# Kernel optimization log

Hardware: AMD Instinct MI355X
Metric: run time of the kernel (lower is better)

Reference implementation:

```python
import jax, jax.numpy as jnp
import numpy as np

HIDDEN_DIM = 2048
CODE_DIM = 256
CODEBOOK_SIZE = 512
FC_DIMS = [1024, 512]
BATCH = 16384
EPS = 1e-5
NEG_SLOPE = 0.01  # PyTorch LeakyReLU default


def _linear_init(key, fan_in, fan_out):
    # kaiming_uniform_(a=sqrt(3)) ~= U(-1/sqrt(fan_in), 1/sqrt(fan_in)) scaled; use uniform bound
    bound = 1.0 / np.sqrt(fan_in)
    return jax.random.uniform(key, (fan_in, fan_out), jnp.float32, -bound, bound)


def setup_inputs() -> dict:
    key = jax.random.key(0)
    ks = jax.random.split(key, 16)
    h = jax.random.normal(ks[0], (BATCH, HIDDEN_DIM), jnp.float32)
    # encoder: Linear(2048->1024, no bias), BN, LReLU, Linear(1024->512, no bias), BN, LReLU, Linear(512->256, bias)
    enc_w1 = _linear_init(ks[1], HIDDEN_DIM, FC_DIMS[0])
    enc_bn1_g = jnp.ones((FC_DIMS[0],), jnp.float32)
    enc_bn1_b = jnp.zeros((FC_DIMS[0],), jnp.float32)
    enc_w2 = _linear_init(ks[2], FC_DIMS[0], FC_DIMS[1])
    enc_bn2_g = jnp.ones((FC_DIMS[1],), jnp.float32)
    enc_bn2_b = jnp.zeros((FC_DIMS[1],), jnp.float32)
    enc_w3 = _linear_init(ks[3], FC_DIMS[1], CODE_DIM)
    enc_b3 = jax.random.uniform(ks[4], (CODE_DIM,), jnp.float32, -1/np.sqrt(FC_DIMS[1]), 1/np.sqrt(FC_DIMS[1]))
    # codebook: NearestEmbed weight shape (code_dim, codebook_size)
    codebook = jax.random.normal(ks[5], (CODE_DIM, CODEBOOK_SIZE), jnp.float32)
    # decoder: Linear(256->512, no bias), BN, LReLU, Linear(512->1024, no bias), BN, LReLU, Linear(1024->2048, bias)
    dec_w1 = _linear_init(ks[6], CODE_DIM, FC_DIMS[1])
    dec_bn1_g = jnp.ones((FC_DIMS[1],), jnp.float32)
    dec_bn1_b = jnp.zeros((FC_DIMS[1],), jnp.float32)
    dec_w2 = _linear_init(ks[7], FC_DIMS[1], FC_DIMS[0])
    dec_bn2_g = jnp.ones((FC_DIMS[0],), jnp.float32)
    dec_bn2_b = jnp.zeros((FC_DIMS[0],), jnp.float32)
    dec_w3 = _linear_init(ks[8], FC_DIMS[0], HIDDEN_DIM)
    dec_b3 = jax.random.uniform(ks[9], (HIDDEN_DIM,), jnp.float32, -1/np.sqrt(FC_DIMS[0]), 1/np.sqrt(FC_DIMS[0]))
    return dict(h=h, enc_w1=enc_w1, enc_bn1_g=enc_bn1_g, enc_bn1_b=enc_bn1_b,
                enc_w2=enc_w2, enc_bn2_g=enc_bn2_g, enc_bn2_b=enc_bn2_b,
                enc_w3=enc_w3, enc_b3=enc_b3, codebook=codebook,
                dec_w1=dec_w1, dec_bn1_g=dec_bn1_g, dec_bn1_b=dec_bn1_b,
                dec_w2=dec_w2, dec_bn2_g=dec_bn2_g, dec_bn2_b=dec_bn2_b,
                dec_w3=dec_w3, dec_b3=dec_b3)


def _bn(x, g, b):
    # BatchNorm1d, training mode: biased batch variance, eps=1e-5
    mu = jnp.mean(x, axis=0)
    var = jnp.var(x, axis=0)
    return (x - mu) * jax.lax.rsqrt(var + EPS) * g + b


def _lrelu(x):
    return jnp.where(x >= 0, x, NEG_SLOPE * x)


def _quantize(z_e, codebook):
    # nearest codebook entry; codebook is [code_dim, K]
    # dist[b,k] = ||z_e[b] - codebook[:,k]||^2 (expanded, drop constant ||z||^2 for argmin? keep full for clarity)
    d = (jnp.sum(z_e * z_e, axis=1, keepdims=True)
         - 2.0 * (z_e @ codebook)
         + jnp.sum(codebook * codebook, axis=0)[None, :])  # [B, K]
    idx = jnp.argmin(d, axis=1)  # [B]
    z_q = codebook.T[idx]        # [B, code_dim]
    return z_q, idx


def reference(h, enc_w1, enc_bn1_g, enc_bn1_b, enc_w2, enc_bn2_g, enc_bn2_b,
              enc_w3, enc_b3, codebook,
              dec_w1, dec_bn1_g, dec_bn1_b, dec_w2, dec_bn2_g, dec_bn2_b,
              dec_w3, dec_b3):
    # encoder
    x = _lrelu(_bn(h @ enc_w1, enc_bn1_g, enc_bn1_b))
    x = _lrelu(_bn(x @ enc_w2, enc_bn2_g, enc_bn2_b))
    z_e = x @ enc_w3 + enc_b3  # [B, code_dim]
    # nearest-embed quantization with straight-through estimator
    z_q_raw, code_indices = _quantize(z_e, codebook)
    z_q = z_e + jax.lax.stop_gradient(z_q_raw - z_e)
    # decoder
    y = _lrelu(_bn(z_q @ dec_w1, dec_bn1_g, dec_bn1_b))
    y = _lrelu(_bn(y @ dec_w2, dec_bn2_g, dec_bn2_b))
    h_recon = y @ dec_w3 + dec_b3  # [B, hidden_dim]
    return z_e, z_q, h_recon, code_indices
```

## Files before the change

kernel.cpp:

```cpp
#include <hip/hip_runtime.h>
#include <hip/hip_fp16.h>
#include <cstdint>
#include <cstddef>

typedef _Float16 f16;
typedef _Float16 half8 __attribute__((ext_vector_type(8)));
typedef _Float16 half4 __attribute__((ext_vector_type(4)));
typedef float floatx4 __attribute__((ext_vector_type(4)));

static constexpr size_t NB  = 16384;
static constexpr size_t DH  = 2048;
static constexpr size_t F1  = 1024;
static constexpr size_t F2  = 512;
static constexpr size_t CD  = 256;
static constexpr size_t KCB = 512;

static constexpr size_t ZE_OFF  = 0;
static constexpr size_t ZQ_OFF  = NB * CD;
static constexpr size_t HR_OFF  = 2 * NB * CD;
static constexpr size_t IDX_OFF = 2 * NB * CD + NB * DH;

static constexpr size_t O_HH   = 0;
static constexpr size_t O_HL   = O_HH + NB * DH * 2;
static constexpr size_t R1_END = O_HL + NB * DH * 2;

static constexpr size_t R_X1H = 0;
static constexpr size_t R_X1L = NB * F1 * 2;
static constexpr size_t R_X2F = 2 * NB * F1 * 2;
static constexpr size_t R_X2H = R_X2F + NB * F2 * 4;
static constexpr size_t R_X2L = R_X2H + NB * F2 * 2;
static constexpr size_t R_Y1F = 0;
static constexpr size_t R_Y1H = NB * F2 * 4;
static constexpr size_t R_Y2H = 0;

static constexpr size_t O_W1H = R1_END;
static constexpr size_t O_W1L = O_W1H + F1 * DH * 2;
static constexpr size_t O_W2H = O_W1L + F1 * DH * 2;
static constexpr size_t O_W2L = O_W2H + F2 * F1 * 2;
static constexpr size_t O_W3H = O_W2L + F2 * F1 * 2;
static constexpr size_t O_W3L = O_W3H + CD * F2 * 2;
static constexpr size_t O_CBH = O_W3L + CD * F2 * 2;
static constexpr size_t O_CBL = O_CBH + KCB * CD * 2;
static constexpr size_t O_DW1 = O_CBL + KCB * CD * 2;
static constexpr size_t O_DW2 = O_DW1 + F2 * CD * 2;
static constexpr size_t O_DW3 = O_DW2 + F1 * F2 * 2;
static constexpr size_t O_SUM = O_DW3 + DH * F1 * 2;
static constexpr size_t O_SQ  = O_SUM + 4 * 1024 * 8;
static constexpr size_t O_SC  = O_SQ + 4 * 1024 * 8;
static constexpr size_t O_SH  = O_SC + 4 * 1024 * 4;
static constexpr size_t O_CN  = O_SH + 4 * 1024 * 4;
static constexpr size_t R2    = (O_CN + 4096 + 255) & ~(size_t)255;
static constexpr size_t R2_X1F = R2;
static constexpr size_t R2_ZEH = R2;
static constexpr size_t R2_ZEL = R2 + NB * CD * 2;
static constexpr size_t R2_S   = R2 + 2 * NB * CD * 2;
static constexpr size_t R2_ZQH = R2_S + NB * KCB * 4;
static constexpr size_t R2_Y2F = R2;

#define GLLDS(src, dst)                                                          \
    __builtin_amdgcn_global_load_lds(                                            \
        (const __attribute__((address_space(1))) void*)(src),                    \
        (__attribute__((address_space(3))) void*)(dst), 16, 0, 0)

#define VMCNT(n)  asm volatile("s_waitcnt vmcnt(" #n ")" ::: "memory")
#define LGKMCNT0  asm volatile("s_waitcnt lgkmcnt(0)" ::: "memory")

__device__ __forceinline__ void xcd_tile(int gx, int BM, int& row0, int& col0)
{
    int id = blockIdx.x + gx * blockIdx.y;
    const int nwg = gx * gridDim.y;
    id = (id & 7) * (nwg >> 3) + (id >> 3);
    row0 = (id % gx) * BM;
    col0 = (id / gx) * 256;
}

template<int MW, bool BIAS, bool STATS, bool WSPLIT>
__global__ __launch_bounds__(512)
void gemm3_t(const f16* __restrict__ Ah_, const f16* __restrict__ Al_,
             const f16* __restrict__ Bh_, const f16* __restrict__ Bl_,
             float* __restrict__ C, const float* __restrict__ bias,
             double* __restrict__ ssum, double* __restrict__ ssq,
             f16* __restrict__ zeh, f16* __restrict__ zel,
             int M, int N, int K)
{
    constexpr int BM = MW * 32;
    __shared__ f16 lds[2][2][16384];
    const int tid  = threadIdx.x;
    const int lane = tid & 63;
    const int w    = tid >> 6;
    const int wr   = w >> 2, wn = w & 3;
    int row0, col0;
    xcd_tile(gridDim.x, BM, row0, col0);

    const int rr8 = lane >> 3;
    const int p   = (lane & 7) ^ rr8;
    const int rr  = w * 32 + rr8;
    const int arr = rr & (BM - 1);
    const f16* srcH = (p < 4) ? (Ah_ + (size_t)(row0 + arr) * K + p * 8)
                              : (Bh_ + (size_t)(col0 + rr) * K + (p - 4) * 8);
    const f16* srcL = (p < 4) ? (Al_ + (size_t)(row0 + arr) * K + p * 8)
                              : (Bl_ + (size_t)(col0 + rr) * K + (p - 4) * 8);
    const int dstBase = w * 32 * 64;
    const int KT = K >> 5;

    floatx4 acc[MW][4];
#pragma unroll
    for (int m = 0; m < MW; ++m)
#pragma unroll
        for (int n = 0; n < 4; ++n)
#pragma unroll
            for (int j = 0; j < 4; ++j) acc[m][n][j] = 0.f;

    const int l15 = lane & 15;
    const int sA  = lane >> 4;

#pragma unroll
    for (int j = 0; j < 4; ++j)
        GLLDS(srcH + (size_t)j * 8 * K, &lds[0][0][dstBase + j * 512]);
#pragma unroll
    for (int j = 0; j < 4; ++j)
        GLLDS(srcL + (size_t)j * 8 * K, &lds[0][1][dstBase + j * 512]);
    VMCNT(4);
    __builtin_amdgcn_s_barrier();

    half8 afh[MW], afl[MW], bfh[4], bfl[4];

    for (int kt = 0; kt < KT; ++kt) {
        const int cur = kt & 1, nxt = cur ^ 1;
        const int koff = (kt + 1 < KT ? kt + 1 : kt) << 5;
        const f16* plH = lds[cur][0];
        const f16* plL = lds[cur][1];

#pragma unroll
        for (int m = 0; m < MW; ++m) {
            const int rA = wr * (MW * 16) + m * 16 + l15;
            afh[m] = *(const half8*)(plH + rA * 64 + (((sA) ^ (rA & 7)) << 3));
        }
#pragma unroll
        for (int n = 0; n < 4; ++n) {
            const int rB = wn * 64 + n * 16 + l15;
            bfh[n] = *(const half8*)(plH + rB * 64 + (((4 + sA) ^ (rB & 7)) << 3));
        }
#pragma unroll
        for (int j = 0; j < 4; ++j)
            GLLDS(srcH + (size_t)j * 8 * K + koff, &lds[nxt][0][dstBase + j * 512]);
        LGKMCNT0;
        __builtin_amdgcn_sched_barrier(0);
        __builtin_amdgcn_s_setprio(1);
#pragma unroll
        for (int m = 0; m < MW; ++m)
#pragma unroll
            for (int n = 0; n < 4; ++n)
                acc[m][n] = __builtin_amdgcn_mfma_f32_16x16x32_f16(afh[m], bfh[n], acc[m][n], 0, 0, 0);
        __builtin_amdgcn_s_setprio(0);
        VMCNT(4);
        __builtin_amdgcn_s_barrier();

#pragma unroll
        for (int n = 0; n < 4; ++n) {
            const int rB = wn * 64 + n * 16 + l15;
            bfl[n] = *(const half8*)(plL + rB * 64 + (((4 + sA) ^ (rB & 7)) << 3));
        }
#pragma unroll
        for (int m = 0; m < MW; ++m) {
            const int rA = wr * (MW * 16) + m * 16 + l15;
            afl[m] = *(const half8*)(plL + rA * 64 + (((sA) ^ (rA & 7)) << 3));
        }
#pragma unroll
        for (int j = 0; j < 4; ++j)
            GLLDS(srcL + (size_t)j * 8 * K + koff, &lds[nxt][1][dstBase + j * 512]);
        LGKMCNT0;
        __builtin_amdgcn_sched_barrier(0);
        __builtin_amdgcn_s_setprio(1);
#pragma unroll
        for (int m = 0; m < MW; ++m)
#pragma unroll
            for (int n = 0; n < 4; ++n)
                acc[m][n] = __builtin_amdgcn_mfma_f32_16x16x32_f16(afh[m], bfl[n], acc[m][n], 0, 0, 0);
#pragma unroll
        for (int m = 0; m < MW; ++m)
#pragma unroll
            for (int n = 0; n < 4; ++n)
                acc[m][n] = __builtin_amdgcn_mfma_f32_16x16x32_f16(afl[m], bfh[n], acc[m][n], 0, 0, 0);
        __builtin_amdgcn_s_setprio(0);
        VMCNT(4);
        __builtin_amdgcn_s_barrier();
    }
    VMCNT(0);

    const int cb0 = col0 + wn * 64;
    const int rb0 = row0 + wr * (MW * 16) + (lane >> 4) * 4;
#pragma unroll
    for (int n = 0; n < 4; ++n) {
        const int col = cb0 + n * 16 + l15;
        const float bv = BIAS ? bias[col] : 0.f;
        double sd = 0.0, sq = 0.0;
#pragma unroll
        for (int m = 0; m < MW; ++m) {
            const int row = rb0 + m * 16;
#pragma unroll
            for (int j = 0; j < 4; ++j) {
                const float v = acc[m][n][j] + bv;
                const size_t o = (size_t)(row + j) * N + col;
                C[o] = v;
                if (WSPLIT) {
                    const f16 hv = (f16)v;
                    zeh[o] = hv;
                    zel[o] = (f16)(v - (float)hv);
                }
                if (STATS) { sd += (double)v; sq += (double)v * (double)v; }
            }
        }
        if (STATS) {
            sd += __shfl_xor(sd, 16);
            sd += __shfl_xor(sd, 32);
            sq += __shfl_xor(sq, 16);
            sq += __shfl_xor(sq, 32);
            if (lane < 16) {
                atomicAdd(ssum + col, sd);
                atomicAdd(ssq + col, sq);
            }
        }
    }
}

template<int MW, bool BIAS, bool STATS>
__global__ __launch_bounds__(512)
void gemm1_t(const f16* __restrict__ A_, const f16* __restrict__ B_,
             float* __restrict__ C, const float* __restrict__ bias,
             double* __restrict__ ssum, double* __restrict__ ssq,
             int M, int N, int K)
{
    constexpr int BM = MW * 32;
    __shared__ f16 lds[3][16384];
    const int tid  = threadIdx.x;
    const int lane = tid & 63;
    const int w    = tid >> 6;
    const int wr   = w >> 2, wn = w & 3;
    int row0, col0;
    xcd_tile(gridDim.x, BM, row0, col0);

    const int rr8 = lane >> 3;
    const int p   = (lane & 7) ^ rr8;
    const int rr  = w * 32 + rr8;
    const int arr = rr & (BM - 1);
    const f16* srcH = (p < 4) ? (A_ + (size_t)(row0 + arr) * K + p * 8)
                              : (B_ + (size_t)(col0 + rr) * K + (p - 4) * 8);
    const int dstBase = w * 32 * 64;
    const int KT = K >> 5;

    floatx4 acc[MW][4];
#pragma unroll
    for (int m = 0; m < MW; ++m)
#pragma unroll
        for (int n = 0; n < 4; ++n)
#pragma unroll
            for (int j = 0; j < 4; ++j) acc[m][n][j] = 0.f;

    const int l15 = lane & 15;
    const int sA  = lane >> 4;

#pragma unroll
    for (int j = 0; j < 4; ++j)
        GLLDS(srcH + (size_t)j * 8 * K, &lds[0][dstBase + j * 512]);
    {
        const int k1 = (KT > 1 ? 1 : 0) << 5;
#pragma unroll
        for (int j = 0; j < 4; ++j)
            GLLDS(srcH + (size_t)j * 8 * K + k1, &lds[1][dstBase + j * 512]);
    }
    VMCNT(4);
    __builtin_amdgcn_s_barrier();

    half8 afh[MW], bfh[4];

    for (int kt = 0; kt < KT; ++kt) {
        const int cur = kt % 3, tgt = (kt + 2) % 3;
        const int koff = (kt + 2 < KT ? kt + 2 : KT - 1) << 5;
        const f16* plH = lds[cur];

#pragma unroll
        for (int m = 0; m < MW; ++m) {
            const int rA = wr * (MW * 16) + m * 16 + l15;
            afh[m] = *(const half8*)(plH + rA * 64 + (((sA) ^ (rA & 7)) << 3));
        }
#pragma unroll
        for (int n = 0; n < 4; ++n) {
            const int rB = wn * 64 + n * 16 + l15;
            bfh[n] = *(const half8*)(plH + rB * 64 + (((4 + sA) ^ (rB & 7)) << 3));
        }
#pragma unroll
        for (int j = 0; j < 4; ++j)
            GLLDS(srcH + (size_t)j * 8 * K + koff, &lds[tgt][dstBase + j * 512]);
        LGKMCNT0;
        __builtin_amdgcn_sched_barrier(0);
        __builtin_amdgcn_s_setprio(1);
#pragma unroll
        for (int m = 0; m < MW; ++m)
#pragma unroll
            for (int n = 0; n < 4; ++n)
                acc[m][n] = __builtin_amdgcn_mfma_f32_16x16x32_f16(afh[m], bfh[n], acc[m][n], 0, 0, 0);
        __builtin_amdgcn_s_setprio(0);
        VMCNT(4);
        __builtin_amdgcn_s_barrier();
    }
    VMCNT(0);

    const int cb0 = col0 + wn * 64;
    const int rb0 = row0 + wr * (MW * 16) + (lane >> 4) * 4;
#pragma unroll
    for (int n = 0; n < 4; ++n) {
        const int col = cb0 + n * 16 + l15;
        const float bv = BIAS ? bias[col] : 0.f;
        double sd = 0.0, sq = 0.0;
#pragma unroll
        for (int m = 0; m < MW; ++m) {
            const int row = rb0 + m * 16;
#pragma unroll
            for (int j = 0; j < 4; ++j) {
                const float v = acc[m][n][j] + bv;
                C[(size_t)(row + j) * N + col] = v;
                if (STATS) { sd += (double)v; sq += (double)v * (double)v; }
            }
        }
        if (STATS) {
            sd += __shfl_xor(sd, 16);
            sd += __shfl_xor(sd, 32);
            sq += __shfl_xor(sq, 16);
            sq += __shfl_xor(sq, 32);
            if (lane < 16) {
                atomicAdd(ssum + col, sd);
                atomicAdd(ssq + col, sq);
            }
        }
    }
}

__global__ void split_f32(const float* __restrict__ X, f16* __restrict__ hi,
                          f16* __restrict__ lo, size_t n4)
{
    const size_t stride = (size_t)gridDim.x * blockDim.x;
    for (size_t i = (size_t)blockIdx.x * blockDim.x + threadIdx.x; i < n4; i += stride) {
        const floatx4 x = ((const floatx4*)X)[i];
        half4 h, l;
#pragma unroll
        for (int j = 0; j < 4; ++j) {
            const float v = x[j];
            const f16 hv = (f16)v;
            h[j] = hv;
            l[j] = (f16)(v - (float)hv);
        }
        ((half4*)hi)[i] = h;
        ((half4*)lo)[i] = l;
    }
}

template<bool SPLIT>
__global__ void bn_apply(const float* __restrict__ X, const float* __restrict__ scale,
                         const float* __restrict__ shift, f16* __restrict__ Yhi,
                         f16* __restrict__ Ylo, size_t n4, int Nmask)
{
    const size_t stride = (size_t)gridDim.x * blockDim.x;
    for (size_t i = (size_t)blockIdx.x * blockDim.x + threadIdx.x; i < n4; i += stride) {
        const floatx4 x = ((const floatx4*)X)[i];
        const int col = (int)((i * 4) & (size_t)Nmask);
        half4 h, l;
#pragma unroll
        for (int j = 0; j < 4; ++j) {
            float v = x[j] * scale[col + j] + shift[col + j];
            v = v >= 0.f ? v : 0.01f * v;
            const f16 hv = (f16)v;
            h[j] = hv;
            if (SPLIT) l[j] = (f16)(v - (float)hv);
        }
        ((half4*)Yhi)[i] = h;
        if (SPLIT) ((half4*)Ylo)[i] = l;
    }
}

__global__ void bn_finalize(const double* __restrict__ ssum, const double* __restrict__ ssq,
                            const float* __restrict__ g, const float* __restrict__ b,
                            float* __restrict__ scale, float* __restrict__ shift, int N)
{
    const int j = blockIdx.x * blockDim.x + threadIdx.x;
    if (j < N) {
        const double inv = 1.0 / (double)NB;
        const double mean = ssum[j] * inv;
        const double var  = ssq[j] * inv - mean * mean;
        const double sc   = (double)g[j] / sqrt(var + 1e-5);
        scale[j] = (float)sc;
        shift[j] = (float)((double)b[j] - mean * sc);
    }
}

template<bool SPLIT>
__global__ void transpose_split(const float* __restrict__ W, f16* __restrict__ Thi,
                                f16* __restrict__ Tlo, int K, int N)
{
    __shared__ float tile[32][33];
    const int x = threadIdx.x;
    const int y = threadIdx.y;
    const int nt = blockIdx.x * 32;
    const int kt = blockIdx.y * 32;
#pragma unroll
    for (int i = 0; i < 32; i += 8)
        tile[y + i][x] = W[(size_t)(kt + y + i) * N + nt + x];
    __syncthreads();
#pragma unroll
    for (int i = 0; i < 32; i += 8) {
        const float v = tile[x][y + i];
        const size_t o = (size_t)(nt + y + i) * K + kt + x;
        const f16 hv = (f16)v;
        Thi[o] = hv;
        if (SPLIT) Tlo[o] = (f16)(v - (float)hv);
    }
}

__global__ void cnorm_kernel(const float* __restrict__ cb, float* __restrict__ cn)
{
    const int k = blockIdx.x * blockDim.x + threadIdx.x;
    if (k < (int)KCB) {
        double s = 0.0;
        for (int d = 0; d < (int)CD; ++d) {
            const float v = cb[(size_t)d * KCB + k];
            s += (double)v * v;
        }
        cn[k] = (float)s;
    }
}

__global__ void argmin_gather(const float* __restrict__ S, const float* __restrict__ cn,
                              const float* __restrict__ cb, float* __restrict__ zq,
                              float* __restrict__ idx_out, f16* __restrict__ zqh)
{
    const int lane = threadIdx.x & 63;
    const int row  = blockIdx.x * 4 + (threadIdx.x >> 6);
    const float* Sr = S + (size_t)row * KCB;
    float best = 3.4e38f;
    int bi = 0;
#pragma unroll
    for (int i = 0; i < 8; ++i) {
        const int k = lane + 64 * i;
        const float d = cn[k] - 2.f * Sr[k];
        if (d < best) { best = d; bi = k; }
    }
#pragma unroll
    for (int off = 32; off > 0; off >>= 1) {
        const float ob = __shfl_xor(best, off);
        const int   oi = __shfl_xor(bi, off);
        if (ob < best || (ob == best && oi < bi)) { best = ob; bi = oi; }
    }
    if (lane == 0) idx_out[row] = (float)bi;
#pragma unroll
    for (int i = 0; i < 4; ++i) {
        const int d = lane + 64 * i;
        const float v = cb[(size_t)d * KCB + bi];
        zq[(size_t)row * CD + d]  = v;
        zqh[(size_t)row * CD + d] = (f16)v;
    }
}

extern "C" void kernel_launch(void* const* d_in, const int* in_sizes, int n_in,
                              void* d_out, int out_size, void* d_ws, size_t ws_size,
                              hipStream_t stream)
{
    (void)in_sizes; (void)n_in; (void)out_size; (void)ws_size;
    const float* h   = (const float*)d_in[0];
    const float* ew1 = (const float*)d_in[1];
    const float* bg1 = (const float*)d_in[2];
    const float* bb1 = (const float*)d_in[3];
    const float* ew2 = (const float*)d_in[4];
    const float* bg2 = (const float*)d_in[5];
    const float* bb2 = (const float*)d_in[6];
    const float* ew3 = (const float*)d_in[7];
    const float* eb3 = (const float*)d_in[8];
    const float* cb  = (const float*)d_in[9];
    const float* dw1 = (const float*)d_in[10];
    const float* dg1 = (const float*)d_in[11];
    const float* db1 = (const float*)d_in[12];
    const float* dw2 = (const float*)d_in[13];
    const float* dg2 = (const float*)d_in[14];
    const float* db2 = (const float*)d_in[15];
    const float* dw3 = (const float*)d_in[16];
    const float* db3 = (const float*)d_in[17];

    char* ws = (char*)d_ws;
    float* out = (float*)d_out;

    f16* Hh  = (f16*)(ws + O_HH);
    f16* Hl  = (f16*)(ws + O_HL);
    f16* W1h = (f16*)(ws + O_W1H);
    f16* W1l = (f16*)(ws + O_W1L);
    f16* W2h = (f16*)(ws + O_W2H);
    f16* W2l = (f16*)(ws + O_W2L);
    f16* W3h = (f16*)(ws + O_W3H);
    f16* W3l = (f16*)(ws + O_W3L);
    f16* CBh = (f16*)(ws + O_CBH);
    f16* CBl = (f16*)(ws + O_CBL);
    f16* D1t = (f16*)(ws + O_DW1);
    f16* D2t = (f16*)(ws + O_DW2);
    f16* D3t = (f16*)(ws + O_DW3);
    double* sum0 = (double*)(ws + O_SUM);
    double* sq0  = (double*)(ws + O_SQ);
    float* sc0 = (float*)(ws + O_SC);
    float* sh0 = (float*)(ws + O_SH);
    float* cn  = (float*)(ws + O_CN);

    float* X1f = (float*)(ws + R2_X1F);
    f16*  X1h = (f16*)(ws + R_X1H);
    f16*  X1l = (f16*)(ws + R_X1L);
    float* X2f = (float*)(ws + R_X2F);
    f16*  X2h = (f16*)(ws + R_X2H);
    f16*  X2l = (f16*)(ws + R_X2L);
    f16*  Zeh = (f16*)(ws + R2_ZEH);
    f16*  Zel = (f16*)(ws + R2_ZEL);
    float* Sb  = (float*)(ws + R2_S);
    f16*  Zqh = (f16*)(ws + R2_ZQH);
    float* Y1f = (float*)(ws + R_Y1F);
    f16*  Y1h = (f16*)(ws + R_Y1H);
    float* Y2f = (float*)(ws + R2_Y2F);
    f16*  Y2h = (f16*)(ws + R_Y2H);

    hipMemsetAsync(ws + O_SUM, 0, 4 * 1024 * 8 * 2, stream);

    split_f32<<<2048, 256, 0, stream>>>(h, Hh, Hl, NB * DH / 4);
    transpose_split<true ><<<dim3(F1 / 32, DH / 32), dim3(32, 8), 0, stream>>>(ew1, W1h, W1l, DH, F1);
    transpose_split<true ><<<dim3(F2 / 32, F1 / 32), dim3(32, 8), 0, stream>>>(ew2, W2h, W2l, F1, F2);
    transpose_split<true ><<<dim3(CD / 32, F2 / 32), dim3(32, 8), 0, stream>>>(ew3, W3h, W3l, F2, CD);
    transpose_split<true ><<<dim3(KCB / 32, CD / 32), dim3(32, 8), 0, stream>>>(cb, CBh, CBl, CD, KCB);
    transpose_split<false><<<dim3(F2 / 32, CD / 32), dim3(32, 8), 0, stream>>>(dw1, D1t, nullptr, CD, F2);
    transpose_split<false><<<dim3(F1 / 32, F2 / 32), dim3(32, 8), 0, stream>>>(dw2, D2t, nullptr, F2, F1);
    transpose_split<false><<<dim3(DH / 32, F1 / 32), dim3(32, 8), 0, stream>>>(dw3, D3t, nullptr, F1, DH);

    gemm3_t<8, false, true, false><<<dim3(NB / 256, F1 / 256), 512, 0, stream>>>(
        Hh, Hl, W1h, W1l, X1f, nullptr, sum0, sq0, nullptr, nullptr, NB, F1, DH);
    bn_finalize<<<4, 256, 0, stream>>>(sum0, sq0, bg1, bb1, sc0, sh0, F1);
    bn_apply<true><<<2048, 256, 0, stream>>>(X1f, sc0, sh0, X1h, X1l, NB * F1 / 4, (int)F1 - 1);

    gemm3_t<4, false, true, false><<<dim3(NB / 128, F2 / 256), 512, 0, stream>>>(
        X1h, X1l, W2h, W2l, X2f, nullptr, sum0 + 1024, sq0 + 1024, nullptr, nullptr, NB, F2, F1);
    bn_finalize<<<2, 256, 0, stream>>>(sum0 + 1024, sq0 + 1024, bg2, bb2, sc0 + 1024, sh0 + 1024, F2);
    bn_apply<true><<<2048, 256, 0, stream>>>(X2f, sc0 + 1024, sh0 + 1024, X2h, X2l, NB * F2 / 4, (int)F2 - 1);

    gemm3_t<4, true, false, true><<<dim3(NB / 128, CD / 256), 512, 0, stream>>>(
        X2h, X2l, W3h, W3l, out + ZE_OFF, eb3, nullptr, nullptr, Zeh, Zel, NB, CD, F2);

    cnorm_kernel<<<2, 256, 0, stream>>>(cb, cn);
    gemm3_t<4, false, false, false><<<dim3(NB / 128, KCB / 256), 512, 0, stream>>>(
        Zeh, Zel, CBh, CBl, Sb, nullptr, nullptr, nullptr, nullptr, nullptr, NB, KCB, CD);
    argmin_gather<<<NB / 4, 256, 0, stream>>>(Sb, cn, cb, out + ZQ_OFF, out + IDX_OFF, Zqh);

    gemm1_t<4, false, true><<<dim3(NB / 128, F2 / 256), 512, 0, stream>>>(
        Zqh, D1t, Y1f, nullptr, sum0 + 2048, sq0 + 2048, NB, F2, CD);
    bn_finalize<<<2, 256, 0, stream>>>(sum0 + 2048, sq0 + 2048, dg1, db1, sc0 + 2048, sh0 + 2048, F2);
    bn_apply<false><<<2048, 256, 0, stream>>>(Y1f, sc0 + 2048, sh0 + 2048, Y1h, nullptr, NB * F2 / 4, (int)F2 - 1);

    gemm1_t<8, false, true><<<dim3(NB / 256, F1 / 256), 512, 0, stream>>>(
        Y1h, D2t, Y2f, nullptr, sum0 + 3072, sq0 + 3072, NB, F1, F2);
    bn_finalize<<<4, 256, 0, stream>>>(sum0 + 3072, sq0 + 3072, dg2, db2, sc0 + 3072, sh0 + 3072, F1);
    bn_apply<false><<<2048, 256, 0, stream>>>(Y2f, sc0 + 3072, sh0 + 3072, Y2h, nullptr, NB * F1 / 4, (int)F1 - 1);

    gemm1_t<8, true, false><<<dim3(NB / 256, DH / 256), 512, 0, stream>>>(
        Y2h, D3t, out + HR_OFF, db3, nullptr, nullptr, NB, DH, F1);
}
```

Measured before the change: 598.4 us.

## Interleave LDS fragment loads with MFMAs and drop XCD tile remapping

Replaces the full lgkmcnt(0) wait before each MFMA block with fine-grained partial waits. The A-fragment LDS reads for later rows are issued while earlier MFMAs run, and the swizzled LDS read offsets are precomputed outside the k-loop. It also removes the XCD-aware workgroup remapping and uses plain blockIdx tiling. The aim is to hide LDS read latency behind MFMA execution. Dropping the XCD remap may hurt L2 locality across chiplets, and the partial-wait logic assumes MW>=2 and that the LDS reads complete in issue order.

```diff
diff --git a/kernel.cpp b/kernel.cpp
--- a/kernel.cpp
+++ b/kernel.cpp
@@ -65,14 +65,16 @@
 #define VMCNT(n)  asm volatile("s_waitcnt vmcnt(" #n ")" ::: "memory")
 #define LGKMCNT0  asm volatile("s_waitcnt lgkmcnt(0)" ::: "memory")
 
-__device__ __forceinline__ void xcd_tile(int gx, int BM, int& row0, int& col0)
-{
-    int id = blockIdx.x + gx * blockIdx.y;
-    const int nwg = gx * gridDim.y;
-    id = (id & 7) * (nwg >> 3) + (id >> 3);
-    row0 = (id % gx) * BM;
-    col0 = (id / gx) * 256;
-}
+#define WAITC(n) do { switch (n) {                                               \
+    case 0: asm volatile("s_waitcnt lgkmcnt(0)" ::: "memory"); break;            \
+    case 1: asm volatile("s_waitcnt lgkmcnt(1)" ::: "memory"); break;            \
+    case 2: asm volatile("s_waitcnt lgkmcnt(2)" ::: "memory"); break;            \
+    case 3: asm volatile("s_waitcnt lgkmcnt(3)" ::: "memory"); break;            \
+    case 4: asm volatile("s_waitcnt lgkmcnt(4)" ::: "memory"); break;            \
+    case 5: asm volatile("s_waitcnt lgkmcnt(5)" ::: "memory"); break;            \
+    case 6: asm volatile("s_waitcnt lgkmcnt(6)" ::: "memory"); break;            \
+    default: asm volatile("s_waitcnt lgkmcnt(7)" ::: "memory"); break; }         \
+    __builtin_amdgcn_sched_barrier(0); } while (0)
 
 template<int MW, bool BIAS, bool STATS, bool WSPLIT>
 __global__ __launch_bounds__(512)
@@ -89,8 +91,8 @@
     const int lane = tid & 63;
     const int w    = tid >> 6;
     const int wr   = w >> 2, wn = w & 3;
-    int row0, col0;
-    xcd_tile(gridDim.x, BM, row0, col0);
+    const int row0 = blockIdx.x * BM;
+    const int col0 = blockIdx.y * 256;
 
     const int rr8 = lane >> 3;
     const int p   = (lane & 7) ^ rr8;
@@ -114,6 +116,18 @@
     const int l15 = lane & 15;
     const int sA  = lane >> 4;
 
+    int rdA[MW], rdB[4];
+#pragma unroll
+    for (int m = 0; m < MW; ++m) {
+        const int rA = wr * (MW * 16) + m * 16 + l15;
+        rdA[m] = rA * 64 + ((sA ^ (rA & 7)) << 3);
+    }
+#pragma unroll
+    for (int n = 0; n < 4; ++n) {
+        const int rB = wn * 64 + n * 16 + l15;
+        rdB[n] = rB * 64 + (((4 + sA) ^ (rB & 7)) << 3);
+    }
+
 #pragma unroll
     for (int j = 0; j < 4; ++j)
         GLLDS(srcH + (size_t)j * 8 * K, &lds[0][0][dstBase + j * 512]);
@@ -132,56 +146,49 @@
         const f16* plL = lds[cur][1];
 
 #pragma unroll
-        for (int m = 0; m < MW; ++m) {
-            const int rA = wr * (MW * 16) + m * 16 + l15;
-            afh[m] = *(const half8*)(plH + rA * 64 + (((sA) ^ (rA & 7)) << 3));
-        }
-#pragma unroll
-        for (int n = 0; n < 4; ++n) {
-            const int rB = wn * 64 + n * 16 + l15;
-            bfh[n] = *(const half8*)(plH + rB * 64 + (((4 + sA) ^ (rB & 7)) << 3));
-        }
+        for (int n = 0; n < 4; ++n) bfh[n] = *(const half8*)(plH + rdB[n]);
+        afh[0] = *(const half8*)(plH + rdA[0]);
+        afh[1] = *(const half8*)(plH + rdA[1]);
 #pragma unroll
         for (int j = 0; j < 4; ++j)
             GLLDS(srcH + (size_t)j * 8 * K + koff, &lds[nxt][0][dstBase + j * 512]);
-        LGKMCNT0;
-        __builtin_amdgcn_sched_barrier(0);
+        WAITC(1);
         __builtin_amdgcn_s_setprio(1);
 #pragma unroll
-        for (int m = 0; m < MW; ++m)
+        for (int m = 0; m < MW; ++m) {
+            if (m + 2 < MW) afh[m + 2] = *(const half8*)(plH + rdA[m + 2]);
 #pragma unroll
             for (int n = 0; n < 4; ++n)
                 acc[m][n] = __builtin_amdgcn_mfma_f32_16x16x32_f16(afh[m], bfh[n], acc[m][n], 0, 0, 0);
+            if (m + 1 < MW) { if (m + 2 < MW) WAITC(1); else WAITC(0); }
+        }
         __builtin_amdgcn_s_setprio(0);
         VMCNT(4);
         __builtin_amdgcn_s_barrier();
 
 #pragma unroll
-        for (int n = 0; n < 4; ++n) {
-            const int rB = wn * 64 + n * 16 + l15;
-            bfl[n] = *(const half8*)(plL + rB * 64 + (((4 + sA) ^ (rB & 7)) << 3));
-        }
-#pragma unroll
-        for (int m = 0; m < MW; ++m) {
-            const int rA = wr * (MW * 16) + m * 16 + l15;
-            afl[m] = *(const half8*)(plL + rA * 64 + (((sA) ^ (rA & 7)) << 3));
-        }
+        for (int n = 0; n < 4; ++n) bfl[n] = *(const half8*)(plL + rdB[n]);
+        afl[0] = *(const half8*)(plL + rdA[0]);
+        afl[1] = *(const half8*)(plL + rdA[1]);
 #pragma unroll
         for (int j = 0; j < 4; ++j)
             GLLDS(srcL + (size_t)j * 8 * K + koff, &lds[nxt][1][dstBase + j * 512]);
-        LGKMCNT0;
-        __builtin_amdgcn_sched_barrier(0);
+        WAITC(2);
         __builtin_amdgcn_s_setprio(1);
 #pragma unroll
-        for (int m = 0; m < MW; ++m)
+        for (int m = 0; m < MW; ++m) {
+            if (m + 2 < MW) afl[m + 2] = *(const half8*)(plL + rdA[m + 2]);
 #pragma unroll
             for (int n = 0; n < 4; ++n)
                 acc[m][n] = __builtin_amdgcn_mfma_f32_16x16x32_f16(afh[m], bfl[n], acc[m][n], 0, 0, 0);
-#pragma unroll
-        for (int m = 0; m < MW; ++m)
+        }
+#pragma unroll
+        for (int m = 0; m < MW; ++m) {
+            WAITC(MW - 1 - m);
 #pragma unroll
             for (int n = 0; n < 4; ++n)
                 acc[m][n] = __builtin_amdgcn_mfma_f32_16x16x32_f16(afl[m], bfh[n], acc[m][n], 0, 0, 0);
+        }
         __builtin_amdgcn_s_setprio(0);
         VMCNT(4);
         __builtin_amdgcn_s_barrier();
@@ -237,8 +244,8 @@
     const int lane = tid & 63;
     const int w    = tid >> 6;
     const int wr   = w >> 2, wn = w & 3;
-    int row0, col0;
-    xcd_tile(gridDim.x, BM, row0, col0);
+    const int row0 = blockIdx.x * BM;
+    const int col0 = blockIdx.y * 256;
 
     const int rr8 = lane >> 3;
     const int p   = (lane & 7) ^ rr8;
@@ -260,6 +267,18 @@
     const int l15 = lane & 15;
     const int sA  = lane >> 4;
 
+    int rdA[MW], rdB[4];
+#pragma unroll
+    for (int m = 0; m < MW; ++m) {
+        const int rA = wr * (MW * 16) + m * 16 + l15;
+        rdA[m] = rA * 64 + ((sA ^ (rA & 7)) << 3);
+    }
+#pragma unroll
+    for (int n = 0; n < 4; ++n) {
+        const int rB = wn * 64 + n * 16 + l15;
+        rdB[n] = rB * 64 + (((4 + sA) ^ (rB & 7)) << 3);
+    }
+
 #pragma unroll
     for (int j = 0; j < 4; ++j)
         GLLDS(srcH + (size_t)j * 8 * K, &lds[0][dstBase + j * 512]);
@@ -280,26 +299,22 @@
         const f16* plH = lds[cur];
 
 #pragma unroll
-        for (int m = 0; m < MW; ++m) {
-            const int rA = wr * (MW * 16) + m * 16 + l15;
-            afh[m] = *(const half8*)(plH + rA * 64 + (((sA) ^ (rA & 7)) << 3));
-        }
-#pragma unroll
-        for (int n = 0; n < 4; ++n) {
-            const int rB = wn * 64 + n * 16 + l15;
-            bfh[n] = *(const half8*)(plH + rB * 64 + (((4 + sA) ^ (rB & 7)) << 3));
-        }
+        for (int n = 0; n < 4; ++n) bfh[n] = *(const half8*)(plH + rdB[n]);
+        afh[0] = *(const half8*)(plH + rdA[0]);
+        afh[1] = *(const half8*)(plH + rdA[1]);
 #pragma unroll
         for (int j = 0; j < 4; ++j)
             GLLDS(srcH + (size_t)j * 8 * K + koff, &lds[tgt][dstBase + j * 512]);
-        LGKMCNT0;
-        __builtin_amdgcn_sched_barrier(0);
+        WAITC(1);
         __builtin_amdgcn_s_setprio(1);
 #pragma unroll
-        for (int m = 0; m < MW; ++m)
+        for (int m = 0; m < MW; ++m) {
+            if (m + 2 < MW) afh[m + 2] = *(const half8*)(plH + rdA[m + 2]);
 #pragma unroll
             for (int n = 0; n < 4; ++n)
                 acc[m][n] = __builtin_amdgcn_mfma_f32_16x16x32_f16(afh[m], bfh[n], acc[m][n], 0, 0, 0);
+            if (m + 1 < MW) { if (m + 2 < MW) WAITC(1); else WAITC(0); }
+        }
         __builtin_amdgcn_s_setprio(0);
         VMCNT(4);
         __builtin_amdgcn_s_barrier();
```

Result: no change. 606.4 us (+1.3%).
